# Kernel tuning notes

Measured on AMD Instinct MI355X. Metric: run time of the kernel, lower is better.

Reference implementation:

```python
import jax, jax.numpy as jnp
import numpy as np

KS = 3          # kernel_size
DIM = 3         # dimension
B, N = 4, 16384
CMAX = 64       # voxel coordinate range [0, CMAX)
K = KS ** DIM   # kernel_volume = 27
SHIFT = KS      # makes neighbor coords non-negative
BASE = CMAX + 2 * KS  # per-axis encoding base


def _kernel_offsets():
    # matches torch: arange(-ks//2 + 1, ks//2 + 1) per dim, meshgrid 'ij'
    r = jnp.arange(-(KS) // 2 + 1, KS // 2 + 1)
    grid = jnp.meshgrid(*([r] * DIM), indexing='ij')
    return jnp.stack(grid, axis=-1).reshape(-1, DIM)  # [K, DIM]


def setup_inputs() -> dict:
    key = jax.random.key(0)
    k1, _ = jax.random.split(key)
    coordinates = jax.random.randint(k1, (B, N, DIM), 0, CMAX, dtype=jnp.int32)
    batch_indices = jnp.broadcast_to(jnp.arange(B, dtype=jnp.int32)[:, None], (B, N))
    return {"coordinates": coordinates, "batch_indices": batch_indices}


def reference(coordinates, batch_indices):
    """Vectorized kernel-map construction (replaces the Python dict-hash loops).

    Returns:
      in_idx  [B*N*K] : index of the input point within its batch
      out_idx [B*N*K] : dense output index (first-appearance order, matches dict insertion)
      rel_pos [B*N*K] : kernel offset index
      out_key [B*N*K, 3] : unique output coordinates, padded with -1 past num_out
      num_out [] : number of valid unique output keys
    """
    Bv, Nv, D = coordinates.shape
    offsets = _kernel_offsets()            # [K, 3]
    Kv = offsets.shape[0]
    # neighbor coordinates, iteration order (b, idx, k) == torch loop order
    nb = coordinates[:, :, None, :] + offsets[None, None, :, :]  # [B, N, K, 3]
    c = nb + SHIFT                                               # non-negative
    b_ids = batch_indices[:, :, None].astype(jnp.int32)
    keys = (b_ids * (BASE ** 3)
            + (c[..., 0] * BASE + c[..., 1]) * BASE + c[..., 2]).reshape(-1)  # [T]
    T = keys.shape[0]
    sentinel = jnp.int32(Bv * (BASE ** 3))  # > any real key
    uniq, first_idx, inv = jnp.unique(keys, size=T, fill_value=sentinel,
                                      return_index=True, return_inverse=True)
    valid = uniq != sentinel
    # recover first-appearance (dict-insertion) order from sorted-unique
    first_adj = jnp.where(valid, first_idx, T)
    order = jnp.argsort(first_adj)                      # insertion order -> sorted pos
    rank = jnp.zeros((T,), dtype=jnp.int32).at[order].set(jnp.arange(T, dtype=jnp.int32))
    out_idx = rank[inv]                                 # [T] dense output indices
    # decode unique keys back to (x, y, z) in insertion order
    uo = uniq[order]
    vo = valid[order]
    rem = uo % (BASE ** 3)
    x = rem // (BASE * BASE) - SHIFT
    y = (rem // BASE) % BASE - SHIFT
    z = rem % BASE - SHIFT
    out_key = jnp.where(vo[:, None], jnp.stack([x, y, z], axis=-1), -1)  # [T, 3]
    num_out = vo.sum()
    in_idx = jnp.tile(jnp.repeat(jnp.arange(Nv, dtype=jnp.int32), Kv), Bv)
    rel_pos = jnp.tile(jnp.arange(Kv, dtype=jnp.int32), Bv * Nv)
    return in_idx, out_idx, rel_pos, out_key, num_out
```

## Files before the change

kernel.cpp:

```cpp
#include <hip/hip_runtime.h>

namespace {
constexpr int Bc   = 4;
constexpr int Nc   = 16384;
constexpr int Kc   = 27;
constexpr int Pc   = 68;
constexpr int P2c  = Pc * Pc;
constexpr int P3c  = Pc * P2c;
constexpr int NPts = Bc * Nc;
constexpr int Tc   = NPts * Kc;
constexpr int FT   = Bc * P3c;
constexpr int PBLKS  = 1024;
constexpr int PPTS   = NPts / PBLKS;
constexpr int OBLKS  = 864;
constexpr int OCHUNK = 8;
}

__device__ __forceinline__ unsigned min3u(unsigned a, unsigned b, unsigned c) {
    return min(min(a, b), c);
}

__global__ void __launch_bounds__(256)
k1_atomic_easy(const int* __restrict__ coords, const int* __restrict__ batch,
               unsigned* __restrict__ cm, unsigned* __restrict__ pcoord,
               int* __restrict__ in_idx, int* __restrict__ rel_pos) {
    const int g = blockIdx.x * 256 + threadIdx.x;
    if (g < NPts) {
        const int bb = batch[g];
        const int x = coords[3 * g], y = coords[3 * g + 1], z = coords[3 * g + 2];
        pcoord[g] = (unsigned)(x | (y << 6) | (z << 12) | (bb << 18));
        atomicMin(&cm[bb * P3c + (x + 2) * P2c + (y + 2) * Pc + (z + 2)],
                  (unsigned)(g & (Nc - 1)));
    }
    const int t = 4 * g;
    int4 a, r;
    a.x = (t / Kc) & (Nc - 1);       r.x = t % Kc;
    a.y = ((t + 1) / Kc) & (Nc - 1); r.y = (t + 1) % Kc;
    a.z = ((t + 2) / Kc) & (Nc - 1); r.z = (t + 2) % Kc;
    a.w = ((t + 3) / Kc) & (Nc - 1); r.w = (t + 3) % Kc;
    reinterpret_cast<int4*>(in_idx)[g]  = a;
    reinterpret_cast<int4*>(rel_pos)[g] = r;
}

__global__ void __launch_bounds__(256)
k3_pred(const unsigned* __restrict__ pcoord, const unsigned* __restrict__ cm,
        unsigned short* __restrict__ owners,
        unsigned long long* __restrict__ packed, int* __restrict__ blockSums) {
    __shared__ int parts[PPTS][4];
    __shared__ int pbs[PPTS];
    __shared__ int scn[256];
    const int tid = threadIdx.x, bid = blockIdx.x;
    const int p = tid >> 2, j = tid & 3;
    const int pt = bid * PPTS + p;

    int mypb = 0;
    if (j < 3) {
        const unsigned pc = pcoord[pt];
        const int x = pc & 63, y = (pc >> 6) & 63, z = (pc >> 12) & 63,
                  bb = pc >> 18;
        const unsigned uidx = (unsigned)(pt & (Nc - 1));
        const unsigned* base0 = cm + bb * P3c + x * P2c + (y + j) * Pc + z;
        unsigned w[5][3];
        #pragma unroll
        for (int xi = 0; xi < 5; ++xi) {
            const unsigned* q = base0 + xi * P2c;
            unsigned rz[3][3];
            #pragma unroll
            for (int yy = 0; yy < 3; ++yy) {
                const unsigned* qq = q + yy * Pc;
                const unsigned v0 = qq[0], v1 = qq[1], v2 = qq[2],
                               v3 = qq[3], v4 = qq[4];
                rz[yy][0] = min3u(v0, v1, v2);
                rz[yy][1] = min3u(v1, v2, v3);
                rz[yy][2] = min3u(v2, v3, v4);
            }
            #pragma unroll
            for (int dz = 0; dz < 3; ++dz)
                w[xi][dz] = min3u(rz[0][dz], rz[1][dz], rz[2][dz]);
        }
        #pragma unroll
        for (int dxl = 0; dxl < 3; ++dxl)
            #pragma unroll
            for (int dz = 0; dz < 3; ++dz) {
                const unsigned m = min3u(w[dxl][dz], w[dxl + 1][dz],
                                         w[dxl + 2][dz]);
                const int kk = (dxl * 3 + j) * 3 + dz;
                owners[pt * Kc + kk] = (unsigned short)m;
                mypb |= (m == uidx) ? (1 << kk) : 0;
            }
    }
    parts[p][j] = mypb;
    __syncthreads();
    if (j == 0) pbs[p] = parts[p][0] | parts[p][1] | parts[p][2];
    __syncthreads();

    const int v = (tid < PPTS) ? __popc(pbs[tid]) : 0;
    scn[tid] = v;
    __syncthreads();
    #pragma unroll
    for (int off = 1; off < PPTS; off <<= 1) {
        int u = (tid >= off) ? scn[tid - off] : 0;
        __syncthreads();
        scn[tid] += u;
        __syncthreads();
    }
    if (tid < PPTS) {
        const int intra = scn[tid] - v;
        packed[bid * PPTS + tid] =
            (unsigned long long)(unsigned)pbs[tid]
          | ((unsigned long long)(unsigned)intra << 27)
          | ((unsigned long long)pcoord[bid * PPTS + tid] << 38);
    }
    if (tid == PPTS - 1) blockSums[bid] = scn[PPTS - 1];
}

__global__ void __launch_bounds__(256)
k4_outputs(const unsigned short* __restrict__ owners,
           const unsigned long long* __restrict__ packed,
           const int* __restrict__ blockSums,
           int* __restrict__ out_idx, int* __restrict__ out_key,
           int* __restrict__ num_out) {
    __shared__ int pref[PBLKS];
    __shared__ int scn[256];
    __shared__ int s_total;
    const int tid = threadIdx.x, bid = blockIdx.x;

    const int4 bsv = reinterpret_cast<const int4*>(blockSums)[tid];
    const int s = bsv.x + bsv.y + bsv.z + bsv.w;
    scn[tid] = s;
    __syncthreads();
    #pragma unroll
    for (int off = 1; off < 256; off <<= 1) {
        int u = (tid >= off) ? scn[tid - off] : 0;
        __syncthreads();
        scn[tid] += u;
        __syncthreads();
    }
    const int excl = scn[tid] - s;
    pref[4 * tid + 0] = excl;
    pref[4 * tid + 1] = excl + bsv.x;
    pref[4 * tid + 2] = excl + bsv.x + bsv.y;
    pref[4 * tid + 3] = excl + bsv.x + bsv.y + bsv.z;
    if (tid == 255) s_total = scn[255];
    __syncthreads();

    const int total = s_total;
    #pragma unroll
    for (int c = 0; c < OCHUNK; ++c) {
        const int t  = bid * (256 * OCHUNK) + c * 256 + tid;
        const int pt = t / Kc;
        const int k  = t - Kc * pt;

        const unsigned long long pkw = packed[pt];
        const int pbw    = (int)(pkw & 0x7ffffffull);
        const int intraw = (int)((pkw >> 27) & 0x7ffull);
        const unsigned pcw = (unsigned)(pkw >> 38);
        const int x = pcw & 63, y = (pcw >> 6) & 63, z = (pcw >> 12) & 63,
                  bb = pcw >> 18;
        const int dx = k / 9 - 1;
        const int dy = (k / 3) % 3 - 1;
        const int dz = k - (k / 3) * 3 - 1;
        const int cx = x + dx, cy = y + dy, cz = z + dz;

        const int o  = (int)owners[t];
        const int go = bb * Nc + o;
        const unsigned long long pko = packed[go];
        const int pbo    = (int)(pko & 0x7ffffffull);
        const int intrao = (int)((pko >> 27) & 0x7ffull);
        const unsigned pco = (unsigned)(pko >> 38);
        const int ox = pco & 63, oy = (pco >> 6) & 63, oz = (pco >> 12) & 63;
        const int kp = (cx - ox + 1) * 9 + (cy - oy + 1) * 3 + (cz - oz + 1);
        out_idx[t] = pref[go >> 6] + intrao + __popc(pbo & ((1 << kp) - 1));

        if ((pbw >> k) & 1) {
            const int r = pref[pt >> 6] + intraw + __popc(pbw & ((1 << k) - 1));
            out_key[3 * r + 0] = cx;
            out_key[3 * r + 1] = cy;
            out_key[3 * r + 2] = cz;
        }
        if (t >= total) {
            out_key[3 * t + 0] = -1;
            out_key[3 * t + 1] = -1;
            out_key[3 * t + 2] = -1;
        }
        if (t == 0) num_out[0] = total;
    }
}

extern "C" void kernel_launch(void* const* d_in, const int* in_sizes, int n_in,
                              void* d_out, int out_size, void* d_ws, size_t ws_size,
                              hipStream_t stream) {
    const int* coords = (const int*)d_in[0];
    const int* batch  = (const int*)d_in[1];
    int* out = (int*)d_out;
    int* in_idx  = out;
    int* out_idx = out + Tc;
    int* rel_pos = out + 2 * Tc;
    int* out_key = out + 3 * Tc;
    int* num_out = out + 6 * Tc;

    unsigned* ws = (unsigned*)d_ws;
    unsigned* cm = ws;
    unsigned long long* packed =
        (unsigned long long*)(ws + FT);
    unsigned short* owners =
        (unsigned short*)(packed + NPts);
    int* blockSums = (int*)(owners + Tc);
    unsigned* pcoord = (unsigned*)(blockSums + PBLKS);

    k1_atomic_easy<<<Tc / 4 / 256, 256, 0, stream>>>(coords, batch, cm, pcoord,
                                                     in_idx, rel_pos);
    k3_pred<<<PBLKS, 256, 0, stream>>>(pcoord, cm, owners, packed, blockSums);
    k4_outputs<<<OBLKS, 256, 0, stream>>>(owners, packed, blockSums,
                                          out_idx, out_key, num_out);
}
```

Measured before the change: 104.9 us.

## Precompute separable y-z min-filter planes in a new kernel; batch loads in output kernel

Adds a k2_planes kernel that computes a 3x3 y-z min filter over the whole occupancy grid in shared memory and writes it to a new table. k3_pred then reads three precomputed values per x-slice instead of 45 raw cells, and only finishes the x-direction min itself. Separately, k4_outputs now issues all owner and packed-record loads for its chunk up front, before the compute loop, to raise memory-level parallelism. The cost is an extra kernel launch plus a full pass over the dense grid and extra workspace, which may not be repaid when points are sparse.

```diff
diff --git a/kernel.cpp b/kernel.cpp
--- a/kernel.cpp
+++ b/kernel.cpp
@@ -10,6 +10,10 @@
 constexpr int NPts = Bc * Nc;
 constexpr int Tc   = NPts * Kc;
 constexpr int FT   = Bc * P3c;
+constexpr unsigned INFu = 0xFFFFFFFFu;
+constexpr int PLANES = Bc * Pc;
+constexpr int SLABS  = 4;
+constexpr int SROWS  = 17;
 constexpr int PBLKS  = 1024;
 constexpr int PPTS   = NPts / PBLKS;
 constexpr int OBLKS  = 864;
@@ -43,7 +47,47 @@
 }
 
 __global__ void __launch_bounds__(256)
-k3_pred(const unsigned* __restrict__ pcoord, const unsigned* __restrict__ cm,
+k2_planes(const unsigned* __restrict__ cm, unsigned* __restrict__ Btab) {
+    __shared__ unsigned s0[(SROWS + 2) * Pc];
+    __shared__ unsigned s1[(SROWS + 2) * Pc];
+    const int tid  = threadIdx.x;
+    const int p    = blockIdx.x / SLABS;
+    const int slab = blockIdx.x - p * SLABS;
+    const int r0   = slab * SROWS;
+    const int base = p * P2c;
+
+    const int n4 = (SROWS + 2) * Pc / 4;
+    for (int i4 = tid; i4 < n4; i4 += 256) {
+        const int li  = 4 * i4;
+        const int row = r0 - 1 + li / Pc;
+        uint4 v = make_uint4(INFu, INFu, INFu, INFu);
+        if (row >= 0 && row < Pc)
+            v = reinterpret_cast<const uint4*>(cm + base + row * Pc)[i4 % (Pc / 4)];
+        reinterpret_cast<uint4*>(s0)[i4] = v;
+    }
+    __syncthreads();
+    for (int i = tid; i < (SROWS + 2) * Pc; i += 256) {
+        const int col = i % Pc;
+        unsigned v = INFu;
+        if (col >= 1 && col <= 66) v = min3u(s0[i - 1], s0[i], s0[i + 1]);
+        s1[i] = v;
+    }
+    __syncthreads();
+    for (int i = tid; i < SROWS * Pc; i += 256) {
+        const int lr  = i / Pc;
+        const int col = i - lr * Pc;
+        const int row = r0 + lr;
+        unsigned v = INFu;
+        if (row >= 1 && row <= 66) {
+            const int li = (lr + 1) * Pc + col;
+            v = min3u(s1[li - Pc], s1[li], s1[li + Pc]);
+        }
+        Btab[base + row * Pc + col] = v;
+    }
+}
+
+__global__ void __launch_bounds__(256)
+k3_pred(const unsigned* __restrict__ pcoord, const unsigned* __restrict__ Btab,
         unsigned short* __restrict__ owners,
         unsigned long long* __restrict__ packed, int* __restrict__ blockSums) {
     __shared__ int parts[PPTS][4];
@@ -59,24 +103,13 @@
         const int x = pc & 63, y = (pc >> 6) & 63, z = (pc >> 12) & 63,
                   bb = pc >> 18;
         const unsigned uidx = (unsigned)(pt & (Nc - 1));
-        const unsigned* base0 = cm + bb * P3c + x * P2c + (y + j) * Pc + z;
+        const unsigned* basep =
+            Btab + bb * P3c + (x * Pc + (y + j + 1)) * Pc + (z + 1);
         unsigned w[5][3];
         #pragma unroll
         for (int xi = 0; xi < 5; ++xi) {
-            const unsigned* q = base0 + xi * P2c;
-            unsigned rz[3][3];
-            #pragma unroll
-            for (int yy = 0; yy < 3; ++yy) {
-                const unsigned* qq = q + yy * Pc;
-                const unsigned v0 = qq[0], v1 = qq[1], v2 = qq[2],
-                               v3 = qq[3], v4 = qq[4];
-                rz[yy][0] = min3u(v0, v1, v2);
-                rz[yy][1] = min3u(v1, v2, v3);
-                rz[yy][2] = min3u(v2, v3, v4);
-            }
-            #pragma unroll
-            for (int dz = 0; dz < 3; ++dz)
-                w[xi][dz] = min3u(rz[0][dz], rz[1][dz], rz[2][dz]);
+            const unsigned* q = basep + xi * P2c;
+            w[xi][0] = q[0]; w[xi][1] = q[1]; w[xi][2] = q[2];
         }
         #pragma unroll
         for (int dxl = 0; dxl < 3; ++dxl)
@@ -145,31 +178,46 @@
     __syncthreads();
 
     const int total = s_total;
+    const int t0 = bid * (256 * OCHUNK) + tid;
+
+    int oo[OCHUNK];
+    #pragma unroll
+    for (int c = 0; c < OCHUNK; ++c) oo[c] = (int)owners[t0 + c * 256];
+
+    int pts[OCHUNK], ks[OCHUNK];
+    unsigned long long pw[OCHUNK], po[OCHUNK];
     #pragma unroll
     for (int c = 0; c < OCHUNK; ++c) {
-        const int t  = bid * (256 * OCHUNK) + c * 256 + tid;
+        const int t  = t0 + c * 256;
         const int pt = t / Kc;
-        const int k  = t - Kc * pt;
-
-        const unsigned long long pkw = packed[pt];
+        pts[c] = pt;
+        ks[c]  = t - Kc * pt;
+        pw[c]  = packed[pt];
+        po[c]  = packed[(pt & ~(Nc - 1)) | oo[c]];
+    }
+
+    #pragma unroll
+    for (int c = 0; c < OCHUNK; ++c) {
+        const int t  = t0 + c * 256;
+        const int pt = pts[c];
+        const int k  = ks[c];
+        const unsigned long long pkw = pw[c];
         const int pbw    = (int)(pkw & 0x7ffffffull);
         const int intraw = (int)((pkw >> 27) & 0x7ffull);
         const unsigned pcw = (unsigned)(pkw >> 38);
-        const int x = pcw & 63, y = (pcw >> 6) & 63, z = (pcw >> 12) & 63,
-                  bb = pcw >> 18;
+        const int x = pcw & 63, y = (pcw >> 6) & 63, z = (pcw >> 12) & 63;
         const int dx = k / 9 - 1;
         const int dy = (k / 3) % 3 - 1;
         const int dz = k - (k / 3) * 3 - 1;
         const int cx = x + dx, cy = y + dy, cz = z + dz;
 
-        const int o  = (int)owners[t];
-        const int go = bb * Nc + o;
-        const unsigned long long pko = packed[go];
+        const unsigned long long pko = po[c];
         const int pbo    = (int)(pko & 0x7ffffffull);
         const int intrao = (int)((pko >> 27) & 0x7ffull);
         const unsigned pco = (unsigned)(pko >> 38);
         const int ox = pco & 63, oy = (pco >> 6) & 63, oz = (pco >> 12) & 63;
         const int kp = (cx - ox + 1) * 9 + (cy - oy + 1) * 3 + (cz - oz + 1);
+        const int go = (pt & ~(Nc - 1)) | oo[c];
         out_idx[t] = pref[go >> 6] + intrao + __popc(pbo & ((1 << kp) - 1));
 
         if ((pbw >> k) & 1) {
@@ -200,9 +248,10 @@
     int* num_out = out + 6 * Tc;
 
     unsigned* ws = (unsigned*)d_ws;
-    unsigned* cm = ws;
+    unsigned* cm   = ws;
+    unsigned* Btab = ws + FT;
     unsigned long long* packed =
-        (unsigned long long*)(ws + FT);
+        (unsigned long long*)(ws + 2 * FT);
     unsigned short* owners =
         (unsigned short*)(packed + NPts);
     int* blockSums = (int*)(owners + Tc);
@@ -210,7 +259,8 @@
 
     k1_atomic_easy<<<Tc / 4 / 256, 256, 0, stream>>>(coords, batch, cm, pcoord,
                                                      in_idx, rel_pos);
-    k3_pred<<<PBLKS, 256, 0, stream>>>(pcoord, cm, owners, packed, blockSums);
+    k2_planes<<<PLANES * SLABS, 256, 0, stream>>>(cm, Btab);
+    k3_pred<<<PBLKS, 256, 0, stream>>>(pcoord, Btab, owners, packed, blockSums);
     k4_outputs<<<OBLKS, 256, 0, stream>>>(owners, packed, blockSums,
                                           out_idx, out_key, num_out);
 }
```

Result: faster. 98.56 us, median of 2 (-6.0%).
